# Performance work log

Measured on AMD Instinct MI355X. Metric: run time of the kernel, lower is better.

The kernel has to match this reference:

```python
import jax, jax.numpy as jnp
import numpy as np

I_T = 0.5       # IoU threshold self.I_t
GAMMA = 2.0     # focal loss gamma
EPS = 1e-7      # focal loss eps clamp
BS, P, C_IN = 8, 2048, 512


def pairwise_iou(b):
    # b: (bs, P, 4) xyxy -> (bs, P, P), same math as torchvision box_iou (no +1)
    area = (b[..., 2] - b[..., 0]) * (b[..., 3] - b[..., 1])
    lt = jnp.maximum(b[:, :, None, :2], b[:, None, :, :2])
    rb = jnp.minimum(b[:, :, None, 2:], b[:, None, :, 2:])
    wh = jnp.clip(rb - lt, 0.0, None)
    inter = wh[..., 0] * wh[..., 1]
    return inter / (area[:, :, None] + area[:, None, :] - inter)


def assign_labels_weights(pre_score, labels, rois):
    # Vectorized, order-faithful version of the per-batch/per-class python loop.
    # Selected seeds per class c: proposals with pre_score[...,c] > 0.5 if more than
    # one, else the single argmax proposal (torch code falls back when k<=1).
    # Sequential `_I > old` running max over (c, j) in ascending order is equivalent
    # to a global first-occurrence argmax (strict >), so per-class max + running
    # compare with earlier-class tie preference reproduces it exactly.
    bs, Pn = pre_score.shape[0], pre_score.shape[1]
    iou = pairwise_iou(rois)                      # (bs, P, P)
    run_I = jnp.full((bs, Pn), -1.0, pre_score.dtype)
    run_w = jnp.ones((bs, Pn), pre_score.dtype)
    hits = []
    for c in range(3):
        s = pre_score[:, :, c]                    # (bs, P)
        th = s > 0.5
        cnt = th.sum(-1)
        onehot = jnp.arange(Pn)[None, :] == jnp.argmax(s, -1)[:, None]
        sel = jnp.where((cnt > 1)[:, None], th, onehot)
        sel = sel & (labels[:, c] != 0)[:, None]  # skip classes absent from image
        masked = jnp.where(sel[:, None, :], iou, -2.0)  # (bs, P, P)
        val = masked.max(-1)                      # best IoU vs any seed of class c
        jidx = masked.argmax(-1)
        cand_x = jnp.take_along_axis(s, jidx, axis=1)
        better = val > run_I
        run_w = jnp.where(better, cand_x, run_w)
        run_I = jnp.where(better, val, run_I)
        hits.append(val > I_T)
    hit = jnp.stack(hits, -1)                     # (bs, P, 3)
    bg = (~hit.any(-1))[..., None]
    y = jnp.concatenate([hit.astype(pre_score.dtype), bg.astype(pre_score.dtype)], -1)
    return y, run_w


def icr_forward(inputs, fc_w, fc_b, pre_score, labels, rois, num):
    bs = inputs.shape[0] // num
    xr = inputs @ fc_w + fc_b                     # (bs*P, 4)
    logit = jax.nn.softmax(xr.reshape(bs, num, 4), -1)
    ps = jax.lax.stop_gradient(pre_score)         # .clone().detach()
    lb = jax.lax.stop_gradient(labels)
    y, w = assign_labels_weights(ps, lb, rois)
    y = y.reshape(bs * num, 4)
    w = w.reshape(bs * num, 1)
    # FocalLoss(gamma=2, mode='none')
    p = jnp.clip(jax.nn.softmax(xr, -1), EPS, 1.0 - EPS)
    fl = -y * jnp.log(p) * (1.0 - p) ** GAMMA
    imbalance = y.sum(0)                          # (4,)
    loss = (w * fl / (imbalance + 1e-7)).reshape(bs, num, 4)
    lab = lb.at[:, 3].set(1.0)[:, None, :]        # lab[:,0,3]=1
    w_ = 10.0 * jnp.exp(logit) * (1.0 - lab) + lab
    loss = (loss * w_).sum() / bs
    return logit, loss


def setup_inputs():
    key = jax.random.key(0)
    k = jax.random.split(key, 6)
    inputs = jax.random.normal(k[0], (BS * P, C_IN), jnp.float32)
    fc_w = jax.random.normal(k[1], (C_IN, 4), jnp.float32) * 0.02
    fc_b = jnp.zeros((4,), jnp.float32)
    pre_score = jax.random.uniform(k[2], (BS, P, 4), dtype=jnp.float32)
    labels = (jax.random.uniform(k[3], (BS, 4)) < 0.5).astype(jnp.float32)
    labels = labels.at[:, 3].set(0.0)
    xy = jax.random.uniform(k[4], (BS, P, 2), dtype=jnp.float32) * 448.0
    wh = jax.random.uniform(k[5], (BS, P, 2), dtype=jnp.float32) * 63.0 + 1.0
    rois = jnp.concatenate([xy, xy + wh], -1)     # valid xyxy boxes in 512x512
    return {"inputs": inputs, "fc_w": fc_w, "fc_b": fc_b, "pre_score": pre_score,
            "labels": labels, "rois": rois, "num": P}


def reference(inputs, fc_w, fc_b, pre_score, labels, rois, num):
    return icr_forward(inputs, fc_w, fc_b, pre_score, labels, rois, num)
```

## Files before the change

kernel.cpp:

```cpp
#include <hip/hip_runtime.h>

#define BSZ 8
#define PN  2048
#define CIN 512
#define CAP 2048
#define NG  64
#define KMAX 768


__global__ __launch_bounds__(256) void k_front(
    const float* __restrict__ inp, const float* __restrict__ fcw,
    const float* __restrict__ fcb, const float* __restrict__ ps,
    const float* __restrict__ labels, const float* __restrict__ rois,
    float* __restrict__ logit, float* __restrict__ accum, int* __restrict__ cnt0,
    int* __restrict__ meta, float* __restrict__ sList,
    float* __restrict__ areaL, float4* __restrict__ roiList)
{
  const int t = threadIdx.x;
  if (blockIdx.x < 1024) {
    const int gw   = (blockIdx.x * 256 + t) >> 6;
    const int lane = t & 63;
    const int kb   = lane << 2;
    const float4 wa0 = *(const float4*)(fcw + (kb + 0) * 4);
    const float4 wa1 = *(const float4*)(fcw + (kb + 1) * 4);
    const float4 wa2 = *(const float4*)(fcw + (kb + 2) * 4);
    const float4 wa3 = *(const float4*)(fcw + (kb + 3) * 4);
    const float4 wb0 = *(const float4*)(fcw + (256 + kb + 0) * 4);
    const float4 wb1 = *(const float4*)(fcw + (256 + kb + 1) * 4);
    const float4 wb2 = *(const float4*)(fcw + (256 + kb + 2) * 4);
    const float4 wb3 = *(const float4*)(fcw + (256 + kb + 3) * 4);
    const float4 bias = *(const float4*)fcb;
    #pragma unroll
    for (int rr = 0; rr < 4; ++rr) {
      const int r = (gw << 2) + rr;
      const float* row = inp + r * CIN;
      const float4 xa = *(const float4*)(row + kb);
      const float4 xb = *(const float4*)(row + 256 + kb);
      float a0 = xa.x*wa0.x + xa.y*wa1.x + xa.z*wa2.x + xa.w*wa3.x
               + xb.x*wb0.x + xb.y*wb1.x + xb.z*wb2.x + xb.w*wb3.x;
      float a1 = xa.x*wa0.y + xa.y*wa1.y + xa.z*wa2.y + xa.w*wa3.y
               + xb.x*wb0.y + xb.y*wb1.y + xb.z*wb2.y + xb.w*wb3.y;
      float a2 = xa.x*wa0.z + xa.y*wa1.z + xa.z*wa2.z + xa.w*wa3.z
               + xb.x*wb0.z + xb.y*wb1.z + xb.z*wb2.z + xb.w*wb3.z;
      float a3 = xa.x*wa0.w + xa.y*wa1.w + xa.z*wa2.w + xa.w*wa3.w
               + xb.x*wb0.w + xb.y*wb1.w + xb.z*wb2.w + xb.w*wb3.w;
      #pragma unroll
      for (int off = 32; off; off >>= 1) {
        a0 += __shfl_xor(a0, off); a1 += __shfl_xor(a1, off);
        a2 += __shfl_xor(a2, off); a3 += __shfl_xor(a3, off);
      }
      if (lane == 0) {
        a0 += bias.x; a1 += bias.y; a2 += bias.z; a3 += bias.w;
        const float m  = fmaxf(fmaxf(a0, a1), fmaxf(a2, a3));
        const float e0 = expf(a0 - m), e1 = expf(a1 - m);
        const float e2 = expf(a2 - m), e3 = expf(a3 - m);
        const float inv = 1.0f / (e0 + e1 + e2 + e3);
        float4 o; o.x = e0*inv; o.y = e1*inv; o.z = e2*inv; o.w = e3*inv;
        *(float4*)(logit + r * 4) = o;
      }
    }
    return;
  }

  const int bc = blockIdx.x - 1024;
  if (bc == 0) {
    if (t < 8) accum[t] = 0.0f;
    if (t == 8) *cnt0 = 0;
  }
  const int b = bc / 3;
  const int c = bc % 3;
  const int j0 = t * 8;

  float sv[8];
  int   flg = 0, cnt = 0;
  float vmax = -1e30f;
  int   jmax = 0;
  #pragma unroll
  for (int m = 0; m < 8; ++m) {
    const float s = ps[(b * PN + j0 + m) * 4 + c];
    sv[m] = s;
    if (s > 0.5f) { flg |= 1 << m; ++cnt; }
    if (s > vmax) { vmax = s; jmax = j0 + m; }
  }

  __shared__ float lv[256];
  __shared__ int   lj[256];
  __shared__ int   pre[256];
  lv[t] = vmax; lj[t] = jmax; pre[t] = cnt;
  __syncthreads();
  for (int off = 128; off > 0; off >>= 1) {
    if (t < off) {
      const float v2 = lv[t + off]; const int j2 = lj[t + off];
      if (v2 > lv[t] || (v2 == lv[t] && j2 < lj[t])) { lv[t] = v2; lj[t] = j2; }
    }
    __syncthreads();
  }
  for (int off = 1; off < 256; off <<= 1) {
    const int add = (t >= off) ? pre[t - off] : 0;
    __syncthreads();
    pre[t] += add;
    __syncthreads();
  }
  const int  totalTh = pre[255];
  const int  excl    = pre[t] - cnt;
  const int  jArg    = lj[0];
  const bool lab     = labels[b * 4 + c] != 0.0f;
  const int  L    = (!lab) ? 0 : ((totalTh > 1) ? totalTh : 1);
  const int  Lpad = (L + 7) & ~7;

  __shared__ float4 lastRoi;
  __shared__ float  lastS, lastA;
  float4* dstR = roiList + bc * CAP;
  float*  dstS = sList   + bc * CAP;
  float*  dstA = areaL   + bc * CAP;
  const float4* rb = ((const float4*)rois) + b * PN;

  if (lab) {
    if (totalTh > 1) {
      int pos = excl;
      #pragma unroll
      for (int m = 0; m < 8; ++m) {
        if (flg & (1 << m)) {
          const float4 r = rb[j0 + m];
          const float  a = (r.z - r.x) * (r.w - r.y);
          dstR[pos] = r; dstS[pos] = sv[m]; dstA[pos] = a;
          if (pos == L - 1) { lastRoi = r; lastS = sv[m]; lastA = a; }
          ++pos;
        }
      }
    } else if (t == (jArg >> 3)) {
      const float4 r = rb[jArg];
      const float  a = (r.z - r.x) * (r.w - r.y);
      dstR[0] = r; dstS[0] = sv[jArg & 7]; dstA[0] = a;
      lastRoi = r; lastS = sv[jArg & 7]; lastA = a;
    }
  }
  __syncthreads();
  if (t < Lpad - L) { dstR[L + t] = lastRoi; dstS[L + t] = lastS; dstA[L + t] = lastA; }
  if (t == 0) meta[bc] = Lpad;
}

__global__ __launch_bounds__(256, 8) void k_assign(
    const float* __restrict__ rois, const int* __restrict__ meta,
    const float4* __restrict__ roiL, const float* __restrict__ areaL,
    float* __restrict__ pbn, float* __restrict__ pbd, int* __restrict__ pbp)
{
  const int g     = blockIdx.x >> 5;
  const int itile = blockIdx.x & 31;
  const int t     = threadIdx.x;
  const int lane  = t & 63;
  const int wv    = t >> 6;

  int P[25];
  P[0] = 0;
  #pragma unroll
  for (int k = 0; k < 24; ++k) P[k + 1] = P[k] + meta[k];
  const int T = P[24];
  const int K = (((T + NG - 1) / NG) + 7) & ~7;
  const int s0 = g * K;
  const int s1 = min(s0 + K, T);
  if (s0 >= s1) return;

  __shared__ float4 sroi[KMAX];
  __shared__ float  sarea[KMAX];
  __shared__ int    spos[KMAX];
  __shared__ float  mrgN[4][64], mrgD[4][64];
  __shared__ int    mrgP[4][64];

  for (int idx = s0 + t; idx < s1; idx += 256) {
    int bcs = 0;
    while (idx >= P[bcs + 1]) ++bcs;
    const int local = idx - P[bcs];
    sroi [idx - s0] = roiL [bcs * CAP + local];
    sarea[idx - s0] = areaL[bcs * CAP + local];
    spos [idx - s0] = local;
  }
  __syncthreads();

  auto upd = [](float& n, float& d, int& p, const float4 ri, const float areai,
                const float4 rj, const float aj, const int pos) {
    const float lx = fmaxf(ri.x, rj.x), ly = fmaxf(ri.y, rj.y);
    const float rx = fminf(ri.z, rj.z), ry = fminf(ri.w, rj.w);
    const float ww = fmaxf(rx - lx, 0.0f), hh = fmaxf(ry - ly, 0.0f);
    const float inter = ww * hh;
    const float uni   = areai + aj - inter;
    if (inter * d > n * uni) { n = inter; d = uni; p = pos; }
  };

  int idx = s0;
  int bc = 0;
  while (idx >= P[bc + 1]) ++bc;
  int curB = -1;
  float4 ri = make_float4(0.f, 0.f, 0.f, 0.f);
  float areai = 0.f;

  while (idx < s1) {
    const int e = min(s1, P[bc + 1]);
    const int b = bc / 3;
    if (b != curB) {
      ri = ((const float4*)rois)[b * PN + (itile << 6) + lane];
      areai = (ri.z - ri.x) * (ri.w - ri.y);
      curB = b;
    }
    const int len = e - idx;
    const int C   = ((len + 31) >> 5) << 3;
    const int o0  = (idx - s0) + wv * C;
    int o1 = o0 + C;
    const int oe = e - s0;
    if (o1 > oe) o1 = oe;

    float nA = -2.0f, dA = 1.0f, nB = -2.0f, dB = 1.0f;
    int   pA = 0, pB = 0;
    for (int o = o0; o < o1; o += 4) {
      const float4 r0 = sroi[o],  r1 = sroi[o+1], r2 = sroi[o+2], r3 = sroi[o+3];
      const float  a0 = sarea[o], a1 = sarea[o+1], a2 = sarea[o+2], a3 = sarea[o+3];
      const int    q0 = spos[o],  q1 = spos[o+1],  q2 = spos[o+2],  q3 = spos[o+3];
      upd(nA, dA, pA, ri, areai, r0, a0, q0);
      upd(nB, dB, pB, ri, areai, r2, a2, q2);
      upd(nA, dA, pA, ri, areai, r1, a1, q1);
      upd(nB, dB, pB, ri, areai, r3, a3, q3);
    }
    { const float xB = nB * dA, xA = nA * dB;
      if (xB > xA || (xB == xA && pB < pA)) { nA = nB; dA = dB; pA = pB; } }

    __syncthreads();
    mrgN[wv][lane] = nA; mrgD[wv][lane] = dA; mrgP[wv][lane] = pA;
    __syncthreads();
    if (wv == 0) {
      float n = mrgN[0][lane], d = mrgD[0][lane]; int p = mrgP[0][lane];
      #pragma unroll
      for (int w = 1; w < 4; ++w) {
        const float n2 = mrgN[w][lane], d2 = mrgD[w][lane];
        const int   p2 = mrgP[w][lane];
        const float x2 = n2 * d, x1 = n * d2;
        if (x2 > x1 || (x2 == x1 && p2 < p)) { n = n2; d = d2; p = p2; }
      }
      const int o = (bc * NG + g) * PN + (itile << 6) + lane;
      pbn[o] = n; pbd[o] = d; pbp[o] = p;
    }
    idx = e; ++bc;
  }
}

__global__ __launch_bounds__(256) void k_back(
    const float* __restrict__ pbn, const float* __restrict__ pbd,
    const int* __restrict__ pbp, const int* __restrict__ meta,
    const float* __restrict__ sList, const float* __restrict__ logit,
    const float* __restrict__ labels, float* __restrict__ accum,
    int* __restrict__ cnt0, float* __restrict__ loss)
{
  const int t  = threadIdx.x;
  const int gi = blockIdx.x * 256 + t;
  const int b  = gi >> 11;
  const int i  = gi & (PN - 1);

  int P[25];
  P[0] = 0;
  #pragma unroll
  for (int k = 0; k < 24; ++k) P[k + 1] = P[k] + meta[k];
  const int T = P[24];
  const int K = (((T + NG - 1) / NG) + 7) & ~7;

  float v[3], sc[3];
  #pragma unroll
  for (int c = 0; c < 3; ++c) {
    const int bc = b * 3 + c;
    const int Pb0 = P[bc], Pb1 = P[bc + 1];
    float n = -2.0f, d = 1.0f; int p = 0;
    if (Pb1 > Pb0) {
      const int gs = Pb0 / K;
      const int ge = (Pb1 + K - 1) / K;
      for (int g = gs; g < ge; ++g) {
        const int o = (bc * NG + g) * PN + i;
        const float n2 = pbn[o], d2 = pbd[o];
        const int   p2 = pbp[o];
        const float x2 = n2 * d, x1 = n * d2;
        if (x2 > x1 || (x2 == x1 && p2 < p)) { n = n2; d = d2; p = p2; }
      }
      v[c]  = n / d;
      sc[c] = sList[bc * CAP + p];
    } else {
      v[c] = -2.0f; sc[c] = 1.0f;
    }
  }
  float runI = -1.0f, runw = 1.0f;
  if (v[0] > runI) { runw = sc[0]; runI = v[0]; }
  if (v[1] > runI) { runw = sc[1]; runI = v[1]; }
  if (v[2] > runI) { runw = sc[2]; runI = v[2]; }
  const float y0 = (v[0] > 0.5f) ? 1.0f : 0.0f;
  const float y1 = (v[1] > 0.5f) ? 1.0f : 0.0f;
  const float y2 = (v[2] > 0.5f) ? 1.0f : 0.0f;
  const float y3 = (y0 + y1 + y2 == 0.0f) ? 1.0f : 0.0f;

  const float4 lg = ((const float4*)logit)[gi];
  const float lb0 = labels[b * 4 + 0];
  const float lb1 = labels[b * 4 + 1];
  const float lb2 = labels[b * 4 + 2];

  auto term = [&](const float l, const float yv, const float labv) -> float {
    const float p2 = fminf(fmaxf(l, 1e-7f), 1.0f - 1e-7f);
    const float om = 1.0f - p2;
    const float fl = -yv * logf(p2) * om * om;
    const float wl = 10.0f * expf(l) * (1.0f - labv) + labv;
    return runw * fl * wl;
  };
  float s[8];
  s[0] = term(lg.x, y0, lb0); s[1] = term(lg.y, y1, lb1);
  s[2] = term(lg.z, y2, lb2); s[3] = term(lg.w, y3, 1.0f);
  s[4] = y0; s[5] = y1; s[6] = y2; s[7] = y3;

  #pragma unroll
  for (int k = 0; k < 8; ++k)
    #pragma unroll
    for (int off = 32; off; off >>= 1) s[k] += __shfl_xor(s[k], off);

  __shared__ float red[4][8];
  const int wv = t >> 6;
  if ((t & 63) == 0)
    #pragma unroll
    for (int k = 0; k < 8; ++k) red[wv][k] = s[k];
  __syncthreads();
  if (t < 8) {
    const float sum = red[0][t] + red[1][t] + red[2][t] + red[3][t];
    atomicAdd(&accum[t], sum);
  }
  __syncthreads();
  if (t == 0) {
    __threadfence();
    if (atomicAdd(cnt0, 1) == 63) {
      float a[8];
      #pragma unroll
      for (int k = 0; k < 8; ++k) a[k] = atomicAdd(&accum[k], 0.0f);
      float L = 0.0f;
      #pragma unroll
      for (int c = 0; c < 4; ++c) L += a[c] / (a[4 + c] + 1e-7f);
      loss[0] = L * 0.125f;
    }
  }
}

extern "C" void kernel_launch(void* const* d_in, const int* in_sizes, int n_in,
                              void* d_out, int out_size, void* d_ws, size_t ws_size,
                              hipStream_t stream)
{
  (void)in_sizes; (void)n_in; (void)out_size; (void)ws_size;
  const float* inp    = (const float*)d_in[0];
  const float* fcw    = (const float*)d_in[1];
  const float* fcb    = (const float*)d_in[2];
  const float* ps     = (const float*)d_in[3];
  const float* labels = (const float*)d_in[4];
  const float* rois   = (const float*)d_in[5];
  float* out = (float*)d_out;

  char* ws = (char*)d_ws;
  float*  accum = (float*) (ws);
  int*    cnt0  = (int*)   (ws + 32);
  int*    meta  = (int*)   (ws + 64);
  float*  sList = (float*) (ws + 1024);
  float*  areaL = (float*) (ws + 197632);
  float4* roiL  = (float4*)(ws + 394240);
  float*  pbn   = (float*) (ws + 1180672);
  float*  pbd   = (float*) (ws + 13763584);
  int*    pbp   = (int*)   (ws + 26346496);

  k_front <<<1048, 256, 0, stream>>>(inp, fcw, fcb, ps, labels, rois,
                                     out, accum, cnt0, meta, sList, areaL, roiL);
  k_assign<<<NG * 32, 256, 0, stream>>>(rois, meta, roiL, areaL, pbn, pbd, pbp);
  k_back  <<<64, 256, 0, stream>>>(pbn, pbd, pbp, meta, sList, out, labels,
                                   accum, cnt0, out + BSZ * PN * 4);
}
```

Before: 123.8 us.

## Split seed selection out, fuse FC into assign kernel, partition seeds per batch

Seed selection now runs as its own small kernel. The FC/softmax work moves into the pairwise-IoU assign kernel as extra blocks, so it overlaps with the IoU scan. The IoU work is repartitioned from 64 global seed-list slices to per-batch quarters (4 per class, all 3 classes in one block), which removes the prefix-sum walk and the per-segment syncs. The partial-result buffers shrink and the back kernel always merges 4 partials. The risk is that a tiny 24-block select kernel now sits serially before the main work, and block-level load balance depends on seed counts per class.

```diff
diff --git a/kernel.cpp b/kernel.cpp
--- a/kernel.cpp
+++ b/kernel.cpp
@@ -4,65 +4,19 @@
 #define PN  2048
 #define CIN 512
 #define CAP 2048
-#define NG  64
-#define KMAX 768
-
-
-__global__ __launch_bounds__(256) void k_front(
-    const float* __restrict__ inp, const float* __restrict__ fcw,
-    const float* __restrict__ fcb, const float* __restrict__ ps,
-    const float* __restrict__ labels, const float* __restrict__ rois,
-    float* __restrict__ logit, float* __restrict__ accum, int* __restrict__ cnt0,
-    int* __restrict__ meta, float* __restrict__ sList,
-    float* __restrict__ areaL, float4* __restrict__ roiList)
+#define NQ  4
+#define KQ  512
+
+
+__global__ __launch_bounds__(256) void k_select(
+    const float* __restrict__ ps, const float* __restrict__ labels,
+    const float* __restrict__ rois, float* __restrict__ accum,
+    int* __restrict__ cnt0, int* __restrict__ meta,
+    float* __restrict__ sList, float* __restrict__ areaL,
+    float4* __restrict__ roiList)
 {
-  const int t = threadIdx.x;
-  if (blockIdx.x < 1024) {
-    const int gw   = (blockIdx.x * 256 + t) >> 6;
-    const int lane = t & 63;
-    const int kb   = lane << 2;
-    const float4 wa0 = *(const float4*)(fcw + (kb + 0) * 4);
-    const float4 wa1 = *(const float4*)(fcw + (kb + 1) * 4);
-    const float4 wa2 = *(const float4*)(fcw + (kb + 2) * 4);
-    const float4 wa3 = *(const float4*)(fcw + (kb + 3) * 4);
-    const float4 wb0 = *(const float4*)(fcw + (256 + kb + 0) * 4);
-    const float4 wb1 = *(const float4*)(fcw + (256 + kb + 1) * 4);
-    const float4 wb2 = *(const float4*)(fcw + (256 + kb + 2) * 4);
-    const float4 wb3 = *(const float4*)(fcw + (256 + kb + 3) * 4);
-    const float4 bias = *(const float4*)fcb;
-    #pragma unroll
-    for (int rr = 0; rr < 4; ++rr) {
-      const int r = (gw << 2) + rr;
-      const float* row = inp + r * CIN;
-      const float4 xa = *(const float4*)(row + kb);
-      const float4 xb = *(const float4*)(row + 256 + kb);
-      float a0 = xa.x*wa0.x + xa.y*wa1.x + xa.z*wa2.x + xa.w*wa3.x
-               + xb.x*wb0.x + xb.y*wb1.x + xb.z*wb2.x + xb.w*wb3.x;
-      float a1 = xa.x*wa0.y + xa.y*wa1.y + xa.z*wa2.y + xa.w*wa3.y
-               + xb.x*wb0.y + xb.y*wb1.y + xb.z*wb2.y + xb.w*wb3.y;
-      float a2 = xa.x*wa0.z + xa.y*wa1.z + xa.z*wa2.z + xa.w*wa3.z
-               + xb.x*wb0.z + xb.y*wb1.z + xb.z*wb2.z + xb.w*wb3.z;
-      float a3 = xa.x*wa0.w + xa.y*wa1.w + xa.z*wa2.w + xa.w*wa3.w
-               + xb.x*wb0.w + xb.y*wb1.w + xb.z*wb2.w + xb.w*wb3.w;
-      #pragma unroll
-      for (int off = 32; off; off >>= 1) {
-        a0 += __shfl_xor(a0, off); a1 += __shfl_xor(a1, off);
-        a2 += __shfl_xor(a2, off); a3 += __shfl_xor(a3, off);
-      }
-      if (lane == 0) {
-        a0 += bias.x; a1 += bias.y; a2 += bias.z; a3 += bias.w;
-        const float m  = fmaxf(fmaxf(a0, a1), fmaxf(a2, a3));
-        const float e0 = expf(a0 - m), e1 = expf(a1 - m);
-        const float e2 = expf(a2 - m), e3 = expf(a3 - m);
-        const float inv = 1.0f / (e0 + e1 + e2 + e3);
-        float4 o; o.x = e0*inv; o.y = e1*inv; o.z = e2*inv; o.w = e3*inv;
-        *(float4*)(logit + r * 4) = o;
-      }
-    }
-    return;
-  }
-
-  const int bc = blockIdx.x - 1024;
+  const int bc = blockIdx.x;
+  const int t  = threadIdx.x;
   if (bc == 0) {
     if (t < 8) accum[t] = 0.0f;
     if (t == 8) *cnt0 = 0;
@@ -140,45 +94,92 @@
   if (t == 0) meta[bc] = Lpad;
 }
 
-__global__ __launch_bounds__(256, 8) void k_assign(
-    const float* __restrict__ rois, const int* __restrict__ meta,
-    const float4* __restrict__ roiL, const float* __restrict__ areaL,
+__global__ __launch_bounds__(256) void k_mega(
+    const float* __restrict__ inp, const float* __restrict__ fcw,
+    const float* __restrict__ fcb, const float* __restrict__ rois,
+    const int* __restrict__ meta, const float4* __restrict__ roiL,
+    const float* __restrict__ areaL, float* __restrict__ logit,
     float* __restrict__ pbn, float* __restrict__ pbd, int* __restrict__ pbp)
 {
-  const int g     = blockIdx.x >> 5;
-  const int itile = blockIdx.x & 31;
-  const int t     = threadIdx.x;
-  const int lane  = t & 63;
-  const int wv    = t >> 6;
-
-  int P[25];
-  P[0] = 0;
-  #pragma unroll
-  for (int k = 0; k < 24; ++k) P[k + 1] = P[k] + meta[k];
-  const int T = P[24];
-  const int K = (((T + NG - 1) / NG) + 7) & ~7;
-  const int s0 = g * K;
-  const int s1 = min(s0 + K, T);
-  if (s0 >= s1) return;
-
-  __shared__ float4 sroi[KMAX];
-  __shared__ float  sarea[KMAX];
-  __shared__ int    spos[KMAX];
-  __shared__ float  mrgN[4][64], mrgD[4][64];
-  __shared__ int    mrgP[4][64];
-
-  for (int idx = s0 + t; idx < s1; idx += 256) {
-    int bcs = 0;
-    while (idx >= P[bcs + 1]) ++bcs;
-    const int local = idx - P[bcs];
-    sroi [idx - s0] = roiL [bcs * CAP + local];
-    sarea[idx - s0] = areaL[bcs * CAP + local];
-    spos [idx - s0] = local;
-  }
-  __syncthreads();
-
-  auto upd = [](float& n, float& d, int& p, const float4 ri, const float areai,
-                const float4 rj, const float aj, const int pos) {
+  const int t    = threadIdx.x;
+  const int lane = t & 63;
+  const int wv   = t >> 6;
+
+  if (blockIdx.x >= 1024) {
+    const int gwv = (blockIdx.x - 1024) * 4 + wv;
+    const int kb  = lane << 2;
+    const float4 wa0 = *(const float4*)(fcw + (kb + 0) * 4);
+    const float4 wa1 = *(const float4*)(fcw + (kb + 1) * 4);
+    const float4 wa2 = *(const float4*)(fcw + (kb + 2) * 4);
+    const float4 wa3 = *(const float4*)(fcw + (kb + 3) * 4);
+    const float4 wb0 = *(const float4*)(fcw + (256 + kb + 0) * 4);
+    const float4 wb1 = *(const float4*)(fcw + (256 + kb + 1) * 4);
+    const float4 wb2 = *(const float4*)(fcw + (256 + kb + 2) * 4);
+    const float4 wb3 = *(const float4*)(fcw + (256 + kb + 3) * 4);
+    const float4 bias = *(const float4*)fcb;
+    #pragma unroll
+    for (int rr = 0; rr < 4; ++rr) {
+      const int r = (gwv << 2) + rr;
+      const float* row = inp + r * CIN;
+      const float4 xa = *(const float4*)(row + kb);
+      const float4 xb = *(const float4*)(row + 256 + kb);
+      float a0 = xa.x*wa0.x + xa.y*wa1.x + xa.z*wa2.x + xa.w*wa3.x
+               + xb.x*wb0.x + xb.y*wb1.x + xb.z*wb2.x + xb.w*wb3.x;
+      float a1 = xa.x*wa0.y + xa.y*wa1.y + xa.z*wa2.y + xa.w*wa3.y
+               + xb.x*wb0.y + xb.y*wb1.y + xb.z*wb2.y + xb.w*wb3.y;
+      float a2 = xa.x*wa0.z + xa.y*wa1.z + xa.z*wa2.z + xa.w*wa3.z
+               + xb.x*wb0.z + xb.y*wb1.z + xb.z*wb2.z + xb.w*wb3.z;
+      float a3 = xa.x*wa0.w + xa.y*wa1.w + xa.z*wa2.w + xa.w*wa3.w
+               + xb.x*wb0.w + xb.y*wb1.w + xb.z*wb2.w + xb.w*wb3.w;
+      #pragma unroll
+      for (int off = 32; off; off >>= 1) {
+        a0 += __shfl_xor(a0, off); a1 += __shfl_xor(a1, off);
+        a2 += __shfl_xor(a2, off); a3 += __shfl_xor(a3, off);
+      }
+      if (lane == 0) {
+        a0 += bias.x; a1 += bias.y; a2 += bias.z; a3 += bias.w;
+        const float m  = fmaxf(fmaxf(a0, a1), fmaxf(a2, a3));
+        const float e0 = expf(a0 - m), e1 = expf(a1 - m);
+        const float e2 = expf(a2 - m), e3 = expf(a3 - m);
+        const float inv = 1.0f / (e0 + e1 + e2 + e3);
+        float4 o; o.x = e0*inv; o.y = e1*inv; o.z = e2*inv; o.w = e3*inv;
+        *(float4*)(logit + r * 4) = o;
+      }
+    }
+    return;
+  }
+
+  const int b     = blockIdx.x >> 7;
+  const int itile = (blockIdx.x >> 2) & 31;
+  const int q     = blockIdx.x & 3;
+
+  __shared__ float4 sroi[3 * KQ];
+  __shared__ float  sarea[3 * KQ];
+  __shared__ float  mrgN[3][4][64];
+  __shared__ float  mrgD[3][4][64];
+  __shared__ int    mrgP[3][4][64];
+
+  int qbase[3], qcnt[3];
+  #pragma unroll
+  for (int c = 0; c < 3; ++c) {
+    const int L  = meta[b * 3 + c];
+    const int K4 = (((L >> 2) + 7) & ~7);
+    const int s0 = q * K4;
+    int e0 = (q + 1) * K4; if (e0 > L) e0 = L;
+    const int cnt = (e0 > s0) ? (e0 - s0) : 0;
+    qbase[c] = s0; qcnt[c] = cnt;
+    for (int o = t; o < cnt; o += 256) {
+      sroi [c * KQ + o] = roiL [(b * 3 + c) * CAP + s0 + o];
+      sarea[c * KQ + o] = areaL[(b * 3 + c) * CAP + s0 + o];
+    }
+  }
+  const int i = (itile << 6) + lane;
+  const float4 ri = ((const float4*)rois)[b * PN + i];
+  const float areai = (ri.z - ri.x) * (ri.w - ri.y);
+  __syncthreads();
+
+  auto upd = [&](float& n, float& d, int& p,
+                 const float4 rj, const float aj, const int pos) {
     const float lx = fmaxf(ri.x, rj.x), ly = fmaxf(ri.y, rj.y);
     const float rx = fminf(ri.z, rj.z), ry = fminf(ri.w, rj.w);
     const float ww = fmaxf(rx - lx, 0.0f), hh = fmaxf(ry - ly, 0.0f);
@@ -187,101 +188,77 @@
     if (inter * d > n * uni) { n = inter; d = uni; p = pos; }
   };
 
-  int idx = s0;
-  int bc = 0;
-  while (idx >= P[bc + 1]) ++bc;
-  int curB = -1;
-  float4 ri = make_float4(0.f, 0.f, 0.f, 0.f);
-  float areai = 0.f;
-
-  while (idx < s1) {
-    const int e = min(s1, P[bc + 1]);
-    const int b = bc / 3;
-    if (b != curB) {
-      ri = ((const float4*)rois)[b * PN + (itile << 6) + lane];
-      areai = (ri.z - ri.x) * (ri.w - ri.y);
-      curB = b;
-    }
-    const int len = e - idx;
-    const int C   = ((len + 31) >> 5) << 3;
-    const int o0  = (idx - s0) + wv * C;
-    int o1 = o0 + C;
-    const int oe = e - s0;
-    if (o1 > oe) o1 = oe;
-
+  float BN[3], BD[3]; int BP[3];
+  #pragma unroll
+  for (int c = 0; c < 3; ++c) {
+    const int cnt = qcnt[c];
+    const int C   = (((cnt + 3) >> 2) + 7) & ~7;
+    const int o0  = wv * C;
+    int o1 = o0 + C; if (o1 > cnt) o1 = cnt;
     float nA = -2.0f, dA = 1.0f, nB = -2.0f, dB = 1.0f;
     int   pA = 0, pB = 0;
+    const float4* rb = sroi  + c * KQ;
+    const float*  ab = sarea + c * KQ;
     for (int o = o0; o < o1; o += 4) {
-      const float4 r0 = sroi[o],  r1 = sroi[o+1], r2 = sroi[o+2], r3 = sroi[o+3];
-      const float  a0 = sarea[o], a1 = sarea[o+1], a2 = sarea[o+2], a3 = sarea[o+3];
-      const int    q0 = spos[o],  q1 = spos[o+1],  q2 = spos[o+2],  q3 = spos[o+3];
-      upd(nA, dA, pA, ri, areai, r0, a0, q0);
-      upd(nB, dB, pB, ri, areai, r2, a2, q2);
-      upd(nA, dA, pA, ri, areai, r1, a1, q1);
-      upd(nB, dB, pB, ri, areai, r3, a3, q3);
+      const float4 r0 = rb[o], r1 = rb[o+1], r2 = rb[o+2], r3 = rb[o+3];
+      const float  a0 = ab[o], a1 = ab[o+1], a2 = ab[o+2], a3 = ab[o+3];
+      upd(nA, dA, pA, r0, a0, o);
+      upd(nB, dB, pB, r2, a2, o + 2);
+      upd(nA, dA, pA, r1, a1, o + 1);
+      upd(nB, dB, pB, r3, a3, o + 3);
     }
     { const float xB = nB * dA, xA = nA * dB;
       if (xB > xA || (xB == xA && pB < pA)) { nA = nB; dA = dB; pA = pB; } }
-
-    __syncthreads();
-    mrgN[wv][lane] = nA; mrgD[wv][lane] = dA; mrgP[wv][lane] = pA;
-    __syncthreads();
-    if (wv == 0) {
-      float n = mrgN[0][lane], d = mrgD[0][lane]; int p = mrgP[0][lane];
+    BN[c] = nA; BD[c] = dA; BP[c] = pA + qbase[c];
+  }
+  #pragma unroll
+  for (int c = 0; c < 3; ++c) {
+    mrgN[c][wv][lane] = BN[c]; mrgD[c][wv][lane] = BD[c]; mrgP[c][wv][lane] = BP[c];
+  }
+  __syncthreads();
+  if (wv == 0) {
+    #pragma unroll
+    for (int c = 0; c < 3; ++c) {
+      float n = BN[c], d = BD[c]; int p = BP[c];
       #pragma unroll
       for (int w = 1; w < 4; ++w) {
-        const float n2 = mrgN[w][lane], d2 = mrgD[w][lane];
-        const int   p2 = mrgP[w][lane];
-        const float x2 = n2 * d, x1 = n * d2;
-        if (x2 > x1 || (x2 == x1 && p2 < p)) { n = n2; d = d2; p = p2; }
+        const float n2 = mrgN[c][w][lane], d2 = mrgD[c][w][lane];
+        const int   p2 = mrgP[c][w][lane];
+        if (n2 * d > n * d2) { n = n2; d = d2; p = p2; }
       }
-      const int o = (bc * NG + g) * PN + (itile << 6) + lane;
+      const int o = ((b * 3 + c) * NQ + q) * PN + i;
       pbn[o] = n; pbd[o] = d; pbp[o] = p;
     }
-    idx = e; ++bc;
   }
 }
 
 __global__ __launch_bounds__(256) void k_back(
     const float* __restrict__ pbn, const float* __restrict__ pbd,
-    const int* __restrict__ pbp, const int* __restrict__ meta,
-    const float* __restrict__ sList, const float* __restrict__ logit,
-    const float* __restrict__ labels, float* __restrict__ accum,
-    int* __restrict__ cnt0, float* __restrict__ loss)
+    const int* __restrict__ pbp, const float* __restrict__ sList,
+    const float* __restrict__ logit, const float* __restrict__ labels,
+    float* __restrict__ accum, int* __restrict__ cnt0,
+    float* __restrict__ loss)
 {
   const int t  = threadIdx.x;
   const int gi = blockIdx.x * 256 + t;
   const int b  = gi >> 11;
   const int i  = gi & (PN - 1);
 
-  int P[25];
-  P[0] = 0;
-  #pragma unroll
-  for (int k = 0; k < 24; ++k) P[k + 1] = P[k] + meta[k];
-  const int T = P[24];
-  const int K = (((T + NG - 1) / NG) + 7) & ~7;
-
   float v[3], sc[3];
   #pragma unroll
   for (int c = 0; c < 3; ++c) {
     const int bc = b * 3 + c;
-    const int Pb0 = P[bc], Pb1 = P[bc + 1];
     float n = -2.0f, d = 1.0f; int p = 0;
-    if (Pb1 > Pb0) {
-      const int gs = Pb0 / K;
-      const int ge = (Pb1 + K - 1) / K;
-      for (int g = gs; g < ge; ++g) {
-        const int o = (bc * NG + g) * PN + i;
-        const float n2 = pbn[o], d2 = pbd[o];
-        const int   p2 = pbp[o];
-        const float x2 = n2 * d, x1 = n * d2;
-        if (x2 > x1 || (x2 == x1 && p2 < p)) { n = n2; d = d2; p = p2; }
-      }
-      v[c]  = n / d;
-      sc[c] = sList[bc * CAP + p];
-    } else {
-      v[c] = -2.0f; sc[c] = 1.0f;
-    }
+    #pragma unroll
+    for (int qq = 0; qq < NQ; ++qq) {
+      const int o = (bc * NQ + qq) * PN + i;
+      const float n2 = pbn[o], d2 = pbd[o];
+      const int   p2 = pbp[o];
+      const float x2 = n2 * d, x1 = n * d2;
+      if (x2 > x1 || (x2 == x1 && p2 < p)) { n = n2; d = d2; p = p2; }
+    }
+    v[c]  = n / d;
+    sc[c] = sList[bc * CAP + p];
   }
   float runI = -1.0f, runw = 1.0f;
   if (v[0] > runI) { runw = sc[0]; runI = v[0]; }
@@ -360,12 +337,13 @@
   float*  areaL = (float*) (ws + 197632);
   float4* roiL  = (float4*)(ws + 394240);
   float*  pbn   = (float*) (ws + 1180672);
-  float*  pbd   = (float*) (ws + 13763584);
-  int*    pbp   = (int*)   (ws + 26346496);
-
-  k_front <<<1048, 256, 0, stream>>>(inp, fcw, fcb, ps, labels, rois,
-                                     out, accum, cnt0, meta, sList, areaL, roiL);
-  k_assign<<<NG * 32, 256, 0, stream>>>(rois, meta, roiL, areaL, pbn, pbd, pbp);
-  k_back  <<<64, 256, 0, stream>>>(pbn, pbd, pbp, meta, sList, out, labels,
-                                   accum, cnt0, out + BSZ * PN * 4);
+  float*  pbd   = (float*) (ws + 1967104);
+  int*    pbp   = (int*)   (ws + 2753536);
+
+  k_select<<<24,   256, 0, stream>>>(ps, labels, rois, accum, cnt0, meta,
+                                     sList, areaL, roiL);
+  k_mega  <<<2048, 256, 0, stream>>>(inp, fcw, fcb, rois, meta, roiL, areaL,
+                                     out, pbn, pbd, pbp);
+  k_back  <<<64,   256, 0, stream>>>(pbn, pbd, pbp, sList, out, labels,
+                                     accum, cnt0, out + BSZ * PN * 4);
 }
```

New measurement: 118.5 us. 1.04x faster.
